# Performance work log

Hardware: AMD Instinct MI355X
Metric: run time of the kernel (lower is better)

The kernel has to match this reference:

```python
import jax, jax.numpy as jnp
import numpy as np
import math

G = 96        # grid cells per axis (domain_size)
N = 400000    # particles, one per occupied cell
CELL = 0.05   # cell size == particle radius parameter d


def setup_inputs():
    rng = np.random.default_rng(0)
    cells = rng.permutation(G ** 3)[:N]
    cz_i = cells // (G * G)
    cy_i = (cells // G) % G
    cx_i = cells % G
    key = jax.random.key(0)
    ks = jax.random.split(key, 6)

    def pos(k, idx):
        jitter = jax.random.uniform(k, (N,), minval=-0.3, maxval=0.3)
        return (jnp.asarray(idx, jnp.float32) + jitter) * CELL

    x = pos(ks[0], cx_i)
    y = pos(ks[1], cy_i)
    z = pos(ks[2], cz_i)
    vx = jax.random.normal(ks[3], (N,), jnp.float32) * 0.1
    vy = jax.random.normal(ks[4], (N,), jnp.float32) * 0.1
    vz = jax.random.normal(ks[5], (N,), jnp.float32) * 0.1
    restitution = 0.5
    alpha = -math.log(restitution) / math.pi
    gamma = alpha / math.sqrt(alpha ** 2 + 1.0)
    kn = 600000.0
    m = 4.0 / 3.0 * 3.1415 * CELL ** 3 * 2700.0
    eta = 2.0 * gamma * math.sqrt(kn * m / 2.0)
    return dict(
        compressed_x_grid=x, compressed_y_grid=y, compressed_z_grid=z,
        compressed_vx_grid=vx, compressed_vy_grid=vy, compressed_vz_grid=vz,
        d=CELL, kn=kn, damping_coefficient_Eta=eta,
        friction_coefficient=0.5, dt=0.001,
        input_shape=(1, 1, G, G, G), filter_size=5)


def reference(compressed_x_grid, compressed_y_grid, compressed_z_grid,
              compressed_vx_grid, compressed_vy_grid, compressed_vz_grid,
              d, kn, damping_coefficient_Eta, friction_coefficient, dt,
              input_shape, filter_size):
    Gz, Gy, Gx = input_shape[2], input_shape[3], input_shape[4]
    n = compressed_x_grid.shape[0]
    eps = jnp.float32(1e-4)
    two_d = 2.0 * d

    # cell indices (one particle per cell, as in the torch module)
    cx = jnp.round(compressed_x_grid / d).astype(jnp.int32)
    cy = jnp.round(compressed_y_grid / d).astype(jnp.int32)
    cz = jnp.round(compressed_z_grid / d).astype(jnp.int32)

    def scatter(v):
        return jnp.zeros((Gz, Gy, Gx), v.dtype).at[cz, cy, cx].set(v)

    xg = scatter(compressed_x_grid)
    yg = scatter(compressed_y_grid)
    zg = scatter(compressed_z_grid)
    vxg = scatter(compressed_vx_grid)
    vyg = scatter(compressed_vy_grid)
    vzg = scatter(compressed_vz_grid)

    half = filter_size // 2
    shifts = jnp.array([[kk - half, jj - half, ii - half]
                        for ii in range(filter_size)
                        for jj in range(filter_size)
                        for kk in range(filter_size)], dtype=jnp.int32)

    def body(carry, shift):
        fxc, fyc, fzc, fxd, fyd, fzd = carry

        def gat(g):
            r = jnp.roll(g, shift[0], axis=0)
            r = jnp.roll(r, shift[1], axis=1)
            r = jnp.roll(r, shift[2], axis=2)
            return r[cz, cy, cx]

        # diff = grid - rolled grid, gathered at the particle cells.
        # grid[cell] holds the particle's own value, so gather(self) == value.
        dx = compressed_x_grid - gat(xg)
        dy = compressed_y_grid - gat(yg)
        dz = compressed_z_grid - gat(zg)
        dvx = compressed_vx_grid - gat(vxg)
        dvy = compressed_vy_grid - gat(vyg)
        dvz = compressed_vz_grid - gat(vzg)

        dist = jnp.sqrt(dx * dx + dy * dy + dz * dz)
        den = jnp.maximum(eps, dist)
        vn = (dvx * dx + dvy * dy + dvz * dz) / den  # normal relative velocity
        ov = dist < two_d                            # overlap mask
        fcol = kn * (dist - two_d) / den             # Hookean repulsion / den
        fdmp = damping_coefficient_Eta * vn / den    # normal damping / den

        fxc = fxc + jnp.where(ov, fcol * dx, 0.0)
        fyc = fyc + jnp.where(ov, fcol * dy, 0.0)
        fzc = fzc + jnp.where(ov, fcol * dz, 0.0)
        fxd = fxd + jnp.where(ov, fdmp * dx, 0.0)
        fyd = fyd + jnp.where(ov, fdmp * dy, 0.0)
        fzd = fzd + jnp.where(ov, fdmp * dz, 0.0)
        return (fxc, fyc, fzc, fxd, fyd, fzd), None

    zeros = jnp.zeros((n,), jnp.float32)
    carry, _ = jax.lax.scan(body, (zeros, zeros, zeros, zeros, zeros, zeros), shifts)
    fxc, fyc, fzc, fxd, fyd, fzd = carry

    # wall (boundary) spring forces, domain extent = grid_dim * cell_size
    dsx, dsy, dsz = Gx * d, Gy * d, Gz * d

    def wall(p, ds):
        lo = jnp.where((p != 0.0) & (p < d), kn * (d - p), 0.0)
        hi = jnp.where(p > ds - two_d, kn * (p - ds + two_d), 0.0)
        return lo - hi

    fbx = wall(compressed_x_grid, dsx)
    fby = wall(compressed_y_grid, dsy)
    fbz = wall(compressed_z_grid, dsz)

    return jnp.stack([fxc, fyc, fzc, fxd, fyd, fzd, fbx, fby, fbz])
```

## Files before the change

### kernel.cpp

```cpp
#include <hip/hip_runtime.h>

#define GDIM 96
#define GCELLS (GDIM * GDIM * GDIM)
#define HX 13
#define HY 12
#define HZ 12
#define HCELLS (HX * HY * HZ)
#define LHC (12 * 12 * 12)
#define TCELLS 512
#define NT 12
#define NBLK (NT * NT * NT)
#define EMPTY32 0xDEDEDEDEu


__global__ __launch_bounds__(256) void scatter_k(
    const float* __restrict__ x, const float* __restrict__ y, const float* __restrict__ z,
    const float* __restrict__ vx, const float* __restrict__ vy, const float* __restrict__ vz,
    const float* __restrict__ dp, const float* __restrict__ knp,
    uint4* __restrict__ grid, float* __restrict__ out, int n)
{
    int i = blockIdx.x * blockDim.x + threadIdx.x;
    if (i >= n) return;
    float d = dp[0], kn = knp[0];
    float invd = 1.0f / d;
    float fx = x[i], fy = y[i], fz = z[i];
    float pxc = fx * invd, pyc = fy * invd, pzc = fz * invd;
    int cx = __float2int_rn(pxc);
    int cy = __float2int_rn(pyc);
    int cz = __float2int_rn(pzc);

    uint4 r0, r1;
    r0.x = __float_as_uint(pxc);
    r0.y = __float_as_uint(pyc);
    r0.z = __float_as_uint(pzc);
    r0.w = __float_as_uint(vx[i]);
    r1.x = __float_as_uint(vy[i]);
    r1.y = __float_as_uint(vz[i]);
    r1.z = 0u;
    r1.w = (unsigned int)(i + 1);
    size_t cell = (size_t)(cz * GDIM + cy) * GDIM + cx;
    grid[2 * cell + 0] = r0;
    grid[2 * cell + 1] = r1;

    float two_d = 2.0f * d, ds = (float)GDIM * d;
    size_t N = (size_t)n;
    float lox = (fx != 0.0f && fx < d) ? kn * (d - fx) : 0.0f;
    float hix = (fx > ds - two_d) ? kn * (fx - ds + two_d) : 0.0f;
    float loy = (fy != 0.0f && fy < d) ? kn * (d - fy) : 0.0f;
    float hiy = (fy > ds - two_d) ? kn * (fy - ds + two_d) : 0.0f;
    float loz = (fz != 0.0f && fz < d) ? kn * (d - fz) : 0.0f;
    float hiz = (fz > ds - two_d) ? kn * (fz - ds + two_d) : 0.0f;
    out[6 * N + i] = lox - hix;
    out[7 * N + i] = loy - hiy;
    out[8 * N + i] = loz - hiz;
}

#define BODY(np, nw) { \
    float dx = xi - np.x, dy = yi - np.y, dz = zi - np.z; \
    float dvx = vxi - np.w, dvy = vyi - nw.x, dvz = vzi - nw.y; \
    float s = fmaf(dx, dx, fmaf(dy, dy, dz * dz)); \
    float t = fmaxf(s, 4e-6f); \
    float rinv = __builtin_amdgcn_rsqf(t); \
    float dist = s * rinv; \
    float dot = fmaf(dvx, dx, fmaf(dvy, dy, dvz * dz)); \
    bool ov = dist < 2.0f; \
    float fc = ov ? (dist - 2.0f) * rinv : 0.0f; \
    float fd = ov ? dot * rinv * rinv : 0.0f; \
    fxc = fmaf(fc, dx, fxc); fyc = fmaf(fc, dy, fyc); fzc = fmaf(fc, dz, fzc); \
    fxd = fmaf(fd, dx, fxd); fyd = fmaf(fd, dy, fyd); fzd = fmaf(fd, dz, fzd); }

#define NROW5(IZ, IY) { int rb = ((lz + IZ) * HY + (ly + IY)) * HX + lx; \
    float4 q0 = P[rb], q1 = P[rb+1], q2 = P[rb+2], q3 = P[rb+3], q4 = P[rb+4]; \
    float2 w0 = Wv[rb], w1 = Wv[rb+1], w2 = Wv[rb+2], w3 = Wv[rb+3], w4 = Wv[rb+4]; \
    BODY(q0, w0) BODY(q1, w1) BODY(q2, w2) BODY(q3, w3) BODY(q4, w4) }
#define NROW3(IZ, IY) { int rb = ((lz + IZ) * HY + (ly + IY)) * HX + lx; \
    float4 q1 = P[rb+1], q2 = P[rb+2], q3 = P[rb+3]; \
    float2 w1 = Wv[rb+1], w2 = Wv[rb+2], w3 = Wv[rb+3]; \
    BODY(q1, w1) BODY(q2, w2) BODY(q3, w3) }
#define NROW1(IZ, IY) { int rb = ((lz + IZ) * HY + (ly + IY)) * HX + lx; \
    float4 q2 = P[rb+2]; float2 w2 = Wv[rb+2]; BODY(q2, w2) }

__global__ __launch_bounds__(512, 6) void force_tile_k(
    const uint4* __restrict__ grid,
    const float* __restrict__ dp, const float* __restrict__ knp,
    const float* __restrict__ etap, float* __restrict__ out, int n)
{
    __shared__ float4 P[HCELLS];
    __shared__ float2 Wv[HCELLS];
    __shared__ float pbuf[6 * 256];
    __shared__ unsigned int llist[TCELLS];
    __shared__ int lcount;

    int tid = threadIdx.x;
    int bid = blockIdx.x;
    int tileid = (bid & 7) * (NBLK / 8) + (bid >> 3);
    int tx = tileid % NT;
    int ty = (tileid / NT) % NT;
    int tz = tileid / (NT * NT);
    int bx = tx * 8 - 2, by = ty * 8 - 2, bz = tz * 8 - 2;

    if (tid == 0) lcount = 0;
    __syncthreads();

    int lane = tid & 63;
    for (int h = tid; h < LHC; h += 512) {
        int hx = h % 12;
        int hy = (h / 12) % 12;
        int hz = h / 144;
        int gx = bx + hx; if (gx < 0) gx += GDIM; else if (gx >= GDIM) gx -= GDIM;
        int gy = by + hy; if (gy < 0) gy += GDIM; else if (gy >= GDIM) gy -= GDIM;
        int gz = bz + hz; if (gz < 0) gz += GDIM; else if (gz >= GDIM) gz -= GDIM;
        size_t gcell = (size_t)(gz * GDIM + gy) * GDIM + gx;
        uint4 r0 = grid[2 * gcell];
        uint4 r1 = grid[2 * gcell + 1];
        int hi = (hz * HY + hy) * HX + hx;
        P[hi] = make_float4(__uint_as_float(r0.x), __uint_as_float(r0.y),
                            __uint_as_float(r0.z), __uint_as_float(r0.w));
        Wv[hi] = make_float2(__uint_as_float(r1.x), __uint_as_float(r1.y));
        bool inter = hx >= 2 && hx < 10 && hy >= 2 && hy < 10 && hz >= 2 && hz < 10;
        bool occ = inter && (r1.w != EMPTY32);
        unsigned long long m = __ballot(occ);
        int base = 0;
        if (lane == 0 && m) base = atomicAdd(&lcount, __popcll(m));
        base = __shfl(base, 0);
        if (occ) {
            int off = __popcll(m & ((1ull << lane) - 1ull));
            int ic = (((hz - 2) * 8 + (hy - 2)) * 8) + (hx - 2);
            llist[base + off] = (r1.w << 9) | (unsigned int)ic;
        }
    }
    __syncthreads();

    float d = dp[0], kn = knp[0], eta = etap[0];
    int cnt = lcount;
    size_t N = (size_t)n;
    int base = tid & 255;
    bool isg0 = tid < 256;
    int nit = (cnt + 255) >> 8;

    for (int it = 0; it < nit; ++it) {
        int ip = it * 256 + base;
        bool act = ip < cnt;
        unsigned int e = llist[act ? ip : 0];
        int lc = (int)(e & 511u);
        int pid = (int)(e >> 9) - 1;
        int lx = lc & 7, ly = (lc >> 3) & 7, lz = lc >> 6;
        int hc = ((lz + 2) * HY + (ly + 2)) * HX + (lx + 2);
        float4 own = P[hc];
        float2 ownw = Wv[hc];
        float xi = own.x, yi = own.y, zi = own.z;
        float vxi = own.w, vyi = ownw.x, vzi = ownw.y;

        float fxc = 0, fyc = 0, fzc = 0, fxd = 0, fyd = 0, fzd = 0;
        if (act) {
            if (isg0) {
                NROW1(0,0) NROW3(0,1) NROW5(0,2) NROW3(0,3) NROW1(0,4)
                NROW3(1,0) NROW5(1,1) NROW5(1,2) NROW5(1,3) NROW3(1,4)
                NROW5(2,0) NROW5(2,1)

                float ss = xi * xi + yi * yi + zi * zi;
                if (ss < 4.0f) {
                    int cntE = 0;
#pragma unroll 1
                    for (int iz = 0; iz < 5; ++iz)
#pragma unroll 1
                        for (int iy = 0; iy < 5; ++iy)
#pragma unroll 1
                            for (int ix = 0; ix < 5; ++ix) {
                                int hc2 = ((lz + iz) * HY + (ly + iy)) * HX + (lx + ix);
                                if (__float_as_uint(P[hc2].x) == EMPTY32) ++cntE;
                            }
                    if (cntE) {
                        float t = fmaxf(ss, 4e-6f);
                        float rinv = __builtin_amdgcn_rsqf(t);
                        float dist = ss * rinv;
                        if (dist < 2.0f) {
                            float fcE = (dist - 2.0f) * rinv;
                            float dotE = vxi * xi + vyi * yi + vzi * zi;
                            float fdE = dotE * rinv * rinv;
                            float c = (float)cntE;
                            fxc = fmaf(c * fcE, xi, fxc); fyc = fmaf(c * fcE, yi, fyc); fzc = fmaf(c * fcE, zi, fzc);
                            fxd = fmaf(c * fdE, xi, fxd); fyd = fmaf(c * fdE, yi, fyd); fzd = fmaf(c * fdE, zi, fzd);
                        }
                    }
                }
            } else {
                NROW5(2,2) NROW5(2,3) NROW5(2,4)
                NROW3(3,0) NROW5(3,1) NROW5(3,2) NROW5(3,3) NROW3(3,4)
                NROW1(4,0) NROW3(4,1) NROW5(4,2) NROW3(4,3) NROW1(4,4)
            }
        }

        __syncthreads();
        if (!isg0 && act) {
            pbuf[0 * 256 + base] = fxc;
            pbuf[1 * 256 + base] = fyc;
            pbuf[2 * 256 + base] = fzc;
            pbuf[3 * 256 + base] = fxd;
            pbuf[4 * 256 + base] = fyd;
            pbuf[5 * 256 + base] = fzd;
        }
        __syncthreads();
        if (isg0 && act) {
            float kd = kn * d;
            out[0 * N + pid] = (fxc + pbuf[0 * 256 + base]) * kd;
            out[1 * N + pid] = (fyc + pbuf[1 * 256 + base]) * kd;
            out[2 * N + pid] = (fzc + pbuf[2 * 256 + base]) * kd;
            out[3 * N + pid] = (fxd + pbuf[3 * 256 + base]) * eta;
            out[4 * N + pid] = (fyd + pbuf[4 * 256 + base]) * eta;
            out[5 * N + pid] = (fzd + pbuf[5 * 256 + base]) * eta;
        }
    }
}

extern "C" void kernel_launch(void* const* d_in, const int* in_sizes, int n_in,
                              void* d_out, int out_size, void* d_ws, size_t ws_size,
                              hipStream_t stream)
{
    const float* x  = (const float*)d_in[0];
    const float* y  = (const float*)d_in[1];
    const float* z  = (const float*)d_in[2];
    const float* vx = (const float*)d_in[3];
    const float* vy = (const float*)d_in[4];
    const float* vz = (const float*)d_in[5];
    const float* dp   = (const float*)d_in[6];
    const float* knp  = (const float*)d_in[7];
    const float* etap = (const float*)d_in[8];
    int n = in_sizes[0];

    uint4* grid = (uint4*)d_ws;

    hipMemsetAsync(d_ws, 0xDE, (size_t)GCELLS * 32, stream);

    int blocks = (n + 255) / 256;
    scatter_k<<<blocks, 256, 0, stream>>>(x, y, z, vx, vy, vz, dp, knp, grid, (float*)d_out, n);
    force_tile_k<<<NBLK, 512, 0, stream>>>(grid, dp, knp, etap, (float*)d_out, n);
}
```

Before: 85.79 us.

## Pack vy/vz as half2, split grid arrays, use one thread per particle

The grid is split into a float4 position+vx array and a uint2 array that holds vy and vz as a half2 plus the particle id. This shrinks the memset, the global traffic and the shared-memory footprint. The force kernel now uses 256 threads, each covering all neighbours of one particle, with loads batched in pairs of rows. That removes the two-half split, the pbuf reduction and its barriers. The half-precision velocities add rounding error to the damping forces, and each thread does twice the serial work.

```diff
diff --git a/kernel.cpp b/kernel.cpp
--- a/kernel.cpp
+++ b/kernel.cpp
@@ -1,4 +1,5 @@
 #include <hip/hip_runtime.h>
+#include <hip/hip_fp16.h>
 
 #define GDIM 96
 #define GCELLS (GDIM * GDIM * GDIM)
@@ -13,11 +14,20 @@
 #define EMPTY32 0xDEDEDEDEu
 
 
+__device__ inline float2 h2f(unsigned int u) {
+    union { unsigned int u; __half2 h; } c; c.u = u;
+    return __half22float2(c.h);
+}
+__device__ inline unsigned int f2h(float a, float b) {
+    union { __half2 h; unsigned int u; } c; c.h = __floats2half2_rn(a, b);
+    return c.u;
+}
+
 __global__ __launch_bounds__(256) void scatter_k(
     const float* __restrict__ x, const float* __restrict__ y, const float* __restrict__ z,
     const float* __restrict__ vx, const float* __restrict__ vy, const float* __restrict__ vz,
     const float* __restrict__ dp, const float* __restrict__ knp,
-    uint4* __restrict__ grid, float* __restrict__ out, int n)
+    float4* __restrict__ Pg, uint2* __restrict__ Vg, float* __restrict__ out, int n)
 {
     int i = blockIdx.x * blockDim.x + threadIdx.x;
     if (i >= n) return;
@@ -29,18 +39,9 @@
     int cy = __float2int_rn(pyc);
     int cz = __float2int_rn(pzc);
 
-    uint4 r0, r1;
-    r0.x = __float_as_uint(pxc);
-    r0.y = __float_as_uint(pyc);
-    r0.z = __float_as_uint(pzc);
-    r0.w = __float_as_uint(vx[i]);
-    r1.x = __float_as_uint(vy[i]);
-    r1.y = __float_as_uint(vz[i]);
-    r1.z = 0u;
-    r1.w = (unsigned int)(i + 1);
     size_t cell = (size_t)(cz * GDIM + cy) * GDIM + cx;
-    grid[2 * cell + 0] = r0;
-    grid[2 * cell + 1] = r1;
+    Pg[cell] = make_float4(pxc, pyc, pzc, vx[i]);
+    Vg[cell] = make_uint2(f2h(vy[i], vz[i]), (unsigned int)(i + 1));
 
     float two_d = 2.0f * d, ds = (float)GDIM * d;
     size_t N = (size_t)n;
@@ -55,7 +56,8 @@
     out[8 * N + i] = loz - hiz;
 }
 
-#define BODY(np, nw) { \
+#define BODY(np, nu) { \
+    float2 nw = h2f(nu); \
     float dx = xi - np.x, dy = yi - np.y, dz = zi - np.z; \
     float dvx = vxi - np.w, dvy = vyi - nw.x, dvz = vzi - nw.y; \
     float s = fmaf(dx, dx, fmaf(dy, dy, dz * dz)); \
@@ -69,25 +71,31 @@
     fxc = fmaf(fc, dx, fxc); fyc = fmaf(fc, dy, fyc); fzc = fmaf(fc, dz, fzc); \
     fxd = fmaf(fd, dx, fxd); fyd = fmaf(fd, dy, fyd); fzd = fmaf(fd, dz, fzd); }
 
-#define NROW5(IZ, IY) { int rb = ((lz + IZ) * HY + (ly + IY)) * HX + lx; \
-    float4 q0 = P[rb], q1 = P[rb+1], q2 = P[rb+2], q3 = P[rb+3], q4 = P[rb+4]; \
-    float2 w0 = Wv[rb], w1 = Wv[rb+1], w2 = Wv[rb+2], w3 = Wv[rb+3], w4 = Wv[rb+4]; \
-    BODY(q0, w0) BODY(q1, w1) BODY(q2, w2) BODY(q3, w3) BODY(q4, w4) }
-#define NROW3(IZ, IY) { int rb = ((lz + IZ) * HY + (ly + IY)) * HX + lx; \
-    float4 q1 = P[rb+1], q2 = P[rb+2], q3 = P[rb+3]; \
-    float2 w1 = Wv[rb+1], w2 = Wv[rb+2], w3 = Wv[rb+3]; \
-    BODY(q1, w1) BODY(q2, w2) BODY(q3, w3) }
-#define NROW1(IZ, IY) { int rb = ((lz + IZ) * HY + (ly + IY)) * HX + lx; \
-    float4 q2 = P[rb+2]; float2 w2 = Wv[rb+2]; BODY(q2, w2) }
-
-__global__ __launch_bounds__(512, 6) void force_tile_k(
-    const uint4* __restrict__ grid,
+#define L5(PF, IZ, IY) \
+    int rb_##PF = ((lz + IZ) * HY + (ly + IY)) * HX + lx; \
+    float4 PF##q0 = P[rb_##PF], PF##q1 = P[rb_##PF+1], PF##q2 = P[rb_##PF+2], \
+           PF##q3 = P[rb_##PF+3], PF##q4 = P[rb_##PF+4]; \
+    unsigned PF##u0 = VV[rb_##PF], PF##u1 = VV[rb_##PF+1], PF##u2 = VV[rb_##PF+2], \
+             PF##u3 = VV[rb_##PF+3], PF##u4 = VV[rb_##PF+4];
+#define B5(PF) BODY(PF##q0, PF##u0) BODY(PF##q1, PF##u1) BODY(PF##q2, PF##u2) \
+               BODY(PF##q3, PF##u3) BODY(PF##q4, PF##u4)
+#define L3(PF, IZ, IY) \
+    int rb_##PF = ((lz + IZ) * HY + (ly + IY)) * HX + lx; \
+    float4 PF##q1 = P[rb_##PF+1], PF##q2 = P[rb_##PF+2], PF##q3 = P[rb_##PF+3]; \
+    unsigned PF##u1 = VV[rb_##PF+1], PF##u2 = VV[rb_##PF+2], PF##u3 = VV[rb_##PF+3];
+#define B3(PF) BODY(PF##q1, PF##u1) BODY(PF##q2, PF##u2) BODY(PF##q3, PF##u3)
+#define L1(PF, IZ, IY) \
+    int rb_##PF = ((lz + IZ) * HY + (ly + IY)) * HX + lx; \
+    float4 PF##q2 = P[rb_##PF+2]; unsigned PF##u2 = VV[rb_##PF+2];
+#define B1(PF) BODY(PF##q2, PF##u2)
+
+__global__ __launch_bounds__(256, 4) void force_tile_k(
+    const float4* __restrict__ Pg, const uint2* __restrict__ Vg,
     const float* __restrict__ dp, const float* __restrict__ knp,
     const float* __restrict__ etap, float* __restrict__ out, int n)
 {
     __shared__ float4 P[HCELLS];
-    __shared__ float2 Wv[HCELLS];
-    __shared__ float pbuf[6 * 256];
+    __shared__ unsigned int VV[HCELLS];
     __shared__ unsigned int llist[TCELLS];
     __shared__ int lcount;
 
@@ -103,7 +111,7 @@
     __syncthreads();
 
     int lane = tid & 63;
-    for (int h = tid; h < LHC; h += 512) {
+    for (int h = tid; h < LHC; h += 256) {
         int hx = h % 12;
         int hy = (h / 12) % 12;
         int hz = h / 144;
@@ -111,14 +119,13 @@
         int gy = by + hy; if (gy < 0) gy += GDIM; else if (gy >= GDIM) gy -= GDIM;
         int gz = bz + hz; if (gz < 0) gz += GDIM; else if (gz >= GDIM) gz -= GDIM;
         size_t gcell = (size_t)(gz * GDIM + gy) * GDIM + gx;
-        uint4 r0 = grid[2 * gcell];
-        uint4 r1 = grid[2 * gcell + 1];
+        float4 r0 = Pg[gcell];
+        uint2 r1 = Vg[gcell];
         int hi = (hz * HY + hy) * HX + hx;
-        P[hi] = make_float4(__uint_as_float(r0.x), __uint_as_float(r0.y),
-                            __uint_as_float(r0.z), __uint_as_float(r0.w));
-        Wv[hi] = make_float2(__uint_as_float(r1.x), __uint_as_float(r1.y));
+        P[hi] = r0;
+        VV[hi] = r1.x;
         bool inter = hx >= 2 && hx < 10 && hy >= 2 && hy < 10 && hz >= 2 && hz < 10;
-        bool occ = inter && (r1.w != EMPTY32);
+        bool occ = inter && (r1.y != EMPTY32);
         unsigned long long m = __ballot(occ);
         int base = 0;
         if (lane == 0 && m) base = atomicAdd(&lcount, __popcll(m));
@@ -126,7 +133,7 @@
         if (occ) {
             int off = __popcll(m & ((1ull << lane) - 1ull));
             int ic = (((hz - 2) * 8 + (hy - 2)) * 8) + (hx - 2);
-            llist[base + off] = (r1.w << 9) | (unsigned int)ic;
+            llist[base + off] = (r1.y << 9) | (unsigned int)ic;
         }
     }
     __syncthreads();
@@ -134,12 +141,10 @@
     float d = dp[0], kn = knp[0], eta = etap[0];
     int cnt = lcount;
     size_t N = (size_t)n;
-    int base = tid & 255;
-    bool isg0 = tid < 256;
     int nit = (cnt + 255) >> 8;
 
     for (int it = 0; it < nit; ++it) {
-        int ip = it * 256 + base;
+        int ip = it * 256 + tid;
         bool act = ip < cnt;
         unsigned int e = llist[act ? ip : 0];
         int lc = (int)(e & 511u);
@@ -147,68 +152,60 @@
         int lx = lc & 7, ly = (lc >> 3) & 7, lz = lc >> 6;
         int hc = ((lz + 2) * HY + (ly + 2)) * HX + (lx + 2);
         float4 own = P[hc];
-        float2 ownw = Wv[hc];
+        float2 ownw = h2f(VV[hc]);
         float xi = own.x, yi = own.y, zi = own.z;
         float vxi = own.w, vyi = ownw.x, vzi = ownw.y;
 
         float fxc = 0, fyc = 0, fzc = 0, fxd = 0, fyd = 0, fzd = 0;
-        if (act) {
-            if (isg0) {
-                NROW1(0,0) NROW3(0,1) NROW5(0,2) NROW3(0,3) NROW1(0,4)
-                NROW3(1,0) NROW5(1,1) NROW5(1,2) NROW5(1,3) NROW3(1,4)
-                NROW5(2,0) NROW5(2,1)
-
-                float ss = xi * xi + yi * yi + zi * zi;
-                if (ss < 4.0f) {
-                    int cntE = 0;
+        { L1(a,0,0) L3(b,0,1) B1(a) B3(b) }
+        { L5(c,0,2) L3(e,0,3) B5(c) B3(e) }
+        { L1(f,0,4) L3(g,1,0) B1(f) B3(g) }
+        { L5(h,1,1) L5(i,1,2) B5(h) B5(i) }
+        { L5(j,1,3) L3(k,1,4) B5(j) B3(k) }
+        { L5(l,2,0) L5(m,2,1) B5(l) B5(m) }
+        { L5(o,2,2) L5(p,2,3) B5(o) B5(p) }
+        { L5(q,2,4) L3(r,3,0) B5(q) B3(r) }
+        { L5(s,3,1) L5(u,3,2) B5(s) B5(u) }
+        { L5(v,3,3) L3(w,3,4) B5(v) B3(w) }
+        { L1(A,4,0) L3(B,4,1) B1(A) B3(B) }
+        { L5(C,4,2) L3(D,4,3) B5(C) B3(D) }
+        { L1(E,4,4) B1(E) }
+
+        float ss = xi * xi + yi * yi + zi * zi;
+        if (act && ss < 4.0f) {
+            int cntE = 0;
 #pragma unroll 1
-                    for (int iz = 0; iz < 5; ++iz)
+            for (int iz = 0; iz < 5; ++iz)
 #pragma unroll 1
-                        for (int iy = 0; iy < 5; ++iy)
+                for (int iy = 0; iy < 5; ++iy)
 #pragma unroll 1
-                            for (int ix = 0; ix < 5; ++ix) {
-                                int hc2 = ((lz + iz) * HY + (ly + iy)) * HX + (lx + ix);
-                                if (__float_as_uint(P[hc2].x) == EMPTY32) ++cntE;
-                            }
-                    if (cntE) {
-                        float t = fmaxf(ss, 4e-6f);
-                        float rinv = __builtin_amdgcn_rsqf(t);
-                        float dist = ss * rinv;
-                        if (dist < 2.0f) {
-                            float fcE = (dist - 2.0f) * rinv;
-                            float dotE = vxi * xi + vyi * yi + vzi * zi;
-                            float fdE = dotE * rinv * rinv;
-                            float c = (float)cntE;
-                            fxc = fmaf(c * fcE, xi, fxc); fyc = fmaf(c * fcE, yi, fyc); fzc = fmaf(c * fcE, zi, fzc);
-                            fxd = fmaf(c * fdE, xi, fxd); fyd = fmaf(c * fdE, yi, fyd); fzd = fmaf(c * fdE, zi, fzd);
-                        }
+                    for (int ix = 0; ix < 5; ++ix) {
+                        int hc2 = ((lz + iz) * HY + (ly + iy)) * HX + (lx + ix);
+                        if (__float_as_uint(P[hc2].x) == EMPTY32) ++cntE;
                     }
+            if (cntE) {
+                float t = fmaxf(ss, 4e-6f);
+                float rinv = __builtin_amdgcn_rsqf(t);
+                float dist = ss * rinv;
+                if (dist < 2.0f) {
+                    float fcE = (dist - 2.0f) * rinv;
+                    float dotE = vxi * xi + vyi * yi + vzi * zi;
+                    float fdE = dotE * rinv * rinv;
+                    float c = (float)cntE;
+                    fxc = fmaf(c * fcE, xi, fxc); fyc = fmaf(c * fcE, yi, fyc); fzc = fmaf(c * fcE, zi, fzc);
+                    fxd = fmaf(c * fdE, xi, fxd); fyd = fmaf(c * fdE, yi, fyd); fzd = fmaf(c * fdE, zi, fzd);
                 }
-            } else {
-                NROW5(2,2) NROW5(2,3) NROW5(2,4)
-                NROW3(3,0) NROW5(3,1) NROW5(3,2) NROW5(3,3) NROW3(3,4)
-                NROW1(4,0) NROW3(4,1) NROW5(4,2) NROW3(4,3) NROW1(4,4)
             }
         }
 
-        __syncthreads();
-        if (!isg0 && act) {
-            pbuf[0 * 256 + base] = fxc;
-            pbuf[1 * 256 + base] = fyc;
-            pbuf[2 * 256 + base] = fzc;
-            pbuf[3 * 256 + base] = fxd;
-            pbuf[4 * 256 + base] = fyd;
-            pbuf[5 * 256 + base] = fzd;
-        }
-        __syncthreads();
-        if (isg0 && act) {
+        if (act) {
             float kd = kn * d;
-            out[0 * N + pid] = (fxc + pbuf[0 * 256 + base]) * kd;
-            out[1 * N + pid] = (fyc + pbuf[1 * 256 + base]) * kd;
-            out[2 * N + pid] = (fzc + pbuf[2 * 256 + base]) * kd;
-            out[3 * N + pid] = (fxd + pbuf[3 * 256 + base]) * eta;
-            out[4 * N + pid] = (fyd + pbuf[4 * 256 + base]) * eta;
-            out[5 * N + pid] = (fzd + pbuf[5 * 256 + base]) * eta;
+            out[0 * N + pid] = fxc * kd;
+            out[1 * N + pid] = fyc * kd;
+            out[2 * N + pid] = fzc * kd;
+            out[3 * N + pid] = fxd * eta;
+            out[4 * N + pid] = fyd * eta;
+            out[5 * N + pid] = fzd * eta;
         }
     }
 }
@@ -228,11 +225,12 @@
     const float* etap = (const float*)d_in[8];
     int n = in_sizes[0];
 
-    uint4* grid = (uint4*)d_ws;
-
-    hipMemsetAsync(d_ws, 0xDE, (size_t)GCELLS * 32, stream);
+    float4* Pg = (float4*)d_ws;
+    uint2* Vg = (uint2*)((char*)d_ws + (size_t)GCELLS * 16);
+
+    hipMemsetAsync(d_ws, 0xDE, (size_t)GCELLS * 24, stream);
 
     int blocks = (n + 255) / 256;
-    scatter_k<<<blocks, 256, 0, stream>>>(x, y, z, vx, vy, vz, dp, knp, grid, (float*)d_out, n);
-    force_tile_k<<<NBLK, 512, 0, stream>>>(grid, dp, knp, etap, (float*)d_out, n);
-}
+    scatter_k<<<blocks, 256, 0, stream>>>(x, y, z, vx, vy, vz, dp, knp, Pg, Vg, (float*)d_out, n);
+    force_tile_k<<<NBLK, 256, 0, stream>>>(Pg, Vg, dp, knp, etap, (float*)d_out, n);
+}
```

After: 184.6 us. +115.1%, slower.

## Use one thread per particle for full stencil and simplify pair math

Applied to the files above, without the earlier changes.

The force kernel changes from two threads per particle, each doing half of the 5x5x5 stencil and combining through shared memory, to one 256-thread block where each thread handles the whole stencil. This removes the pbuf reduction and two barriers per iteration. The self cell is skipped through a new 4-neighbour row macro. The pair math now tests overlap on squared distance and computes the coefficient as 1-2*rinv, dropping the clamp and a multiply. The trade-off is longer serial work per thread and fewer threads in flight. The unclamped rsqrt could produce inf for coincident pairs.

```diff
diff --git a/kernel.cpp b/kernel.cpp
--- a/kernel.cpp
+++ b/kernel.cpp
@@ -59,12 +59,10 @@
     float dx = xi - np.x, dy = yi - np.y, dz = zi - np.z; \
     float dvx = vxi - np.w, dvy = vyi - nw.x, dvz = vzi - nw.y; \
     float s = fmaf(dx, dx, fmaf(dy, dy, dz * dz)); \
-    float t = fmaxf(s, 4e-6f); \
-    float rinv = __builtin_amdgcn_rsqf(t); \
-    float dist = s * rinv; \
+    float rinv = __builtin_amdgcn_rsqf(s); \
     float dot = fmaf(dvx, dx, fmaf(dvy, dy, dvz * dz)); \
-    bool ov = dist < 2.0f; \
-    float fc = ov ? (dist - 2.0f) * rinv : 0.0f; \
+    bool ov = s < 4.0f; \
+    float fc = ov ? fmaf(-2.0f, rinv, 1.0f) : 0.0f; \
     float fd = ov ? dot * rinv * rinv : 0.0f; \
     fxc = fmaf(fc, dx, fxc); fyc = fmaf(fc, dy, fyc); fzc = fmaf(fc, dz, fzc); \
     fxd = fmaf(fd, dx, fxd); fyd = fmaf(fd, dy, fyd); fzd = fmaf(fd, dz, fzd); }
@@ -73,6 +71,10 @@
     float4 q0 = P[rb], q1 = P[rb+1], q2 = P[rb+2], q3 = P[rb+3], q4 = P[rb+4]; \
     float2 w0 = Wv[rb], w1 = Wv[rb+1], w2 = Wv[rb+2], w3 = Wv[rb+3], w4 = Wv[rb+4]; \
     BODY(q0, w0) BODY(q1, w1) BODY(q2, w2) BODY(q3, w3) BODY(q4, w4) }
+#define NROW4S(IZ, IY) { int rb = ((lz + IZ) * HY + (ly + IY)) * HX + lx; \
+    float4 q0 = P[rb], q1 = P[rb+1], q3 = P[rb+3], q4 = P[rb+4]; \
+    float2 w0 = Wv[rb], w1 = Wv[rb+1], w3 = Wv[rb+3], w4 = Wv[rb+4]; \
+    BODY(q0, w0) BODY(q1, w1) BODY(q3, w3) BODY(q4, w4) }
 #define NROW3(IZ, IY) { int rb = ((lz + IZ) * HY + (ly + IY)) * HX + lx; \
     float4 q1 = P[rb+1], q2 = P[rb+2], q3 = P[rb+3]; \
     float2 w1 = Wv[rb+1], w2 = Wv[rb+2], w3 = Wv[rb+3]; \
@@ -80,14 +82,13 @@
 #define NROW1(IZ, IY) { int rb = ((lz + IZ) * HY + (ly + IY)) * HX + lx; \
     float4 q2 = P[rb+2]; float2 w2 = Wv[rb+2]; BODY(q2, w2) }
 
-__global__ __launch_bounds__(512, 6) void force_tile_k(
+__global__ __launch_bounds__(256) void force_tile_k(
     const uint4* __restrict__ grid,
     const float* __restrict__ dp, const float* __restrict__ knp,
     const float* __restrict__ etap, float* __restrict__ out, int n)
 {
     __shared__ float4 P[HCELLS];
     __shared__ float2 Wv[HCELLS];
-    __shared__ float pbuf[6 * 256];
     __shared__ unsigned int llist[TCELLS];
     __shared__ int lcount;
 
@@ -103,7 +104,7 @@
     __syncthreads();
 
     int lane = tid & 63;
-    for (int h = tid; h < LHC; h += 512) {
+    for (int h = tid; h < LHC; h += 256) {
         int hx = h % 12;
         int hy = (h / 12) % 12;
         int hz = h / 144;
@@ -134,12 +135,10 @@
     float d = dp[0], kn = knp[0], eta = etap[0];
     int cnt = lcount;
     size_t N = (size_t)n;
-    int base = tid & 255;
-    bool isg0 = tid < 256;
     int nit = (cnt + 255) >> 8;
 
     for (int it = 0; it < nit; ++it) {
-        int ip = it * 256 + base;
+        int ip = it * 256 + tid;
         bool act = ip < cnt;
         unsigned int e = llist[act ? ip : 0];
         int lc = (int)(e & 511u);
@@ -152,63 +151,47 @@
         float vxi = own.w, vyi = ownw.x, vzi = ownw.y;
 
         float fxc = 0, fyc = 0, fzc = 0, fxd = 0, fyd = 0, fzd = 0;
-        if (act) {
-            if (isg0) {
-                NROW1(0,0) NROW3(0,1) NROW5(0,2) NROW3(0,3) NROW1(0,4)
-                NROW3(1,0) NROW5(1,1) NROW5(1,2) NROW5(1,3) NROW3(1,4)
-                NROW5(2,0) NROW5(2,1)
-
-                float ss = xi * xi + yi * yi + zi * zi;
-                if (ss < 4.0f) {
-                    int cntE = 0;
+        NROW1(0,0) NROW3(0,1) NROW5(0,2) NROW3(0,3) NROW1(0,4)
+        NROW3(1,0) NROW5(1,1) NROW5(1,2) NROW5(1,3) NROW3(1,4)
+        NROW5(2,0) NROW5(2,1) NROW4S(2,2) NROW5(2,3) NROW5(2,4)
+        NROW3(3,0) NROW5(3,1) NROW5(3,2) NROW5(3,3) NROW3(3,4)
+        NROW1(4,0) NROW3(4,1) NROW5(4,2) NROW3(4,3) NROW1(4,4)
+
+        float ss = xi * xi + yi * yi + zi * zi;
+        if (act && ss < 4.0f) {
+            int cntE = 0;
 #pragma unroll 1
-                    for (int iz = 0; iz < 5; ++iz)
+            for (int iz = 0; iz < 5; ++iz)
 #pragma unroll 1
-                        for (int iy = 0; iy < 5; ++iy)
+                for (int iy = 0; iy < 5; ++iy)
 #pragma unroll 1
-                            for (int ix = 0; ix < 5; ++ix) {
-                                int hc2 = ((lz + iz) * HY + (ly + iy)) * HX + (lx + ix);
-                                if (__float_as_uint(P[hc2].x) == EMPTY32) ++cntE;
-                            }
-                    if (cntE) {
-                        float t = fmaxf(ss, 4e-6f);
-                        float rinv = __builtin_amdgcn_rsqf(t);
-                        float dist = ss * rinv;
-                        if (dist < 2.0f) {
-                            float fcE = (dist - 2.0f) * rinv;
-                            float dotE = vxi * xi + vyi * yi + vzi * zi;
-                            float fdE = dotE * rinv * rinv;
-                            float c = (float)cntE;
-                            fxc = fmaf(c * fcE, xi, fxc); fyc = fmaf(c * fcE, yi, fyc); fzc = fmaf(c * fcE, zi, fzc);
-                            fxd = fmaf(c * fdE, xi, fxd); fyd = fmaf(c * fdE, yi, fyd); fzd = fmaf(c * fdE, zi, fzd);
-                        }
+                    for (int ix = 0; ix < 5; ++ix) {
+                        int hc2 = ((lz + iz) * HY + (ly + iy)) * HX + (lx + ix);
+                        if (__float_as_uint(P[hc2].x) == EMPTY32) ++cntE;
                     }
+            if (cntE) {
+                float t = fmaxf(ss, 4e-6f);
+                float rinv = __builtin_amdgcn_rsqf(t);
+                float dist = ss * rinv;
+                if (dist < 2.0f) {
+                    float fcE = (dist - 2.0f) * rinv;
+                    float dotE = vxi * xi + vyi * yi + vzi * zi;
+                    float fdE = dotE * rinv * rinv;
+                    float c = (float)cntE;
+                    fxc = fmaf(c * fcE, xi, fxc); fyc = fmaf(c * fcE, yi, fyc); fzc = fmaf(c * fcE, zi, fzc);
+                    fxd = fmaf(c * fdE, xi, fxd); fyd = fmaf(c * fdE, yi, fyd); fzd = fmaf(c * fdE, zi, fzd);
                 }
-            } else {
-                NROW5(2,2) NROW5(2,3) NROW5(2,4)
-                NROW3(3,0) NROW5(3,1) NROW5(3,2) NROW5(3,3) NROW3(3,4)
-                NROW1(4,0) NROW3(4,1) NROW5(4,2) NROW3(4,3) NROW1(4,4)
             }
         }
 
-        __syncthreads();
-        if (!isg0 && act) {
-            pbuf[0 * 256 + base] = fxc;
-            pbuf[1 * 256 + base] = fyc;
-            pbuf[2 * 256 + base] = fzc;
-            pbuf[3 * 256 + base] = fxd;
-            pbuf[4 * 256 + base] = fyd;
-            pbuf[5 * 256 + base] = fzd;
-        }
-        __syncthreads();
-        if (isg0 && act) {
+        if (act) {
             float kd = kn * d;
-            out[0 * N + pid] = (fxc + pbuf[0 * 256 + base]) * kd;
-            out[1 * N + pid] = (fyc + pbuf[1 * 256 + base]) * kd;
-            out[2 * N + pid] = (fzc + pbuf[2 * 256 + base]) * kd;
-            out[3 * N + pid] = (fxd + pbuf[3 * 256 + base]) * eta;
-            out[4 * N + pid] = (fyd + pbuf[4 * 256 + base]) * eta;
-            out[5 * N + pid] = (fzd + pbuf[5 * 256 + base]) * eta;
+            out[0 * N + pid] = fxc * kd;
+            out[1 * N + pid] = fyc * kd;
+            out[2 * N + pid] = fzc * kd;
+            out[3 * N + pid] = fxd * eta;
+            out[4 * N + pid] = fyd * eta;
+            out[5 * N + pid] = fzd * eta;
         }
     }
 }
@@ -234,5 +217,5 @@
 
     int blocks = (n + 255) / 256;
     scatter_k<<<blocks, 256, 0, stream>>>(x, y, z, vx, vy, vz, dp, knp, grid, (float*)d_out, n);
-    force_tile_k<<<NBLK, 512, 0, stream>>>(grid, dp, knp, etap, (float*)d_out, n);
+    force_tile_k<<<NBLK, 256, 0, stream>>>(grid, dp, knp, etap, (float*)d_out, n);
 }
```

Result: slower. 97.53 us (+13.7%).
